# Optimization experiments

Hardware: AMD Instinct MI355X
Metric: run time of the kernel (lower is better)

Reference implementation:

```python
import jax, jax.numpy as jnp
import numpy as np

B, S, D, H = 8, 2048, 1024, 64

def setup_inputs() -> dict:
    key = jax.random.key(0)
    ks = jax.random.split(key, 7)
    scale = 0.02
    return {
        "x": jax.random.normal(ks[0], (B, S, D), dtype=jnp.float32),
        "Wq": jax.random.normal(ks[1], (D, H), dtype=jnp.float32) * scale,
        "bq": jax.random.normal(ks[2], (H,), dtype=jnp.float32) * scale,
        "Wk": jax.random.normal(ks[3], (D, H), dtype=jnp.float32) * scale,
        "bk": jax.random.normal(ks[4], (H,), dtype=jnp.float32) * scale,
        "Wv": jax.random.normal(ks[5], (D, H), dtype=jnp.float32) * scale,
        "bv": jax.random.normal(ks[6], (H,), dtype=jnp.float32) * scale,
    }

def reference(x, Wq, bq, Wk, bk, Wv, bv):
    # Single-head causal self-attention (dropout in eval mode -> identity).
    q = x @ Wq + bq            # [B,S,H]
    k = x @ Wk + bk            # [B,S,H]
    v = x @ Wv + bv            # [B,S,H]
    scores = jnp.einsum("bqh,bkh->bqk", q, k)  # [B,S,S]
    s = q.shape[1]
    causal = jnp.tril(jnp.ones((s, s), dtype=bool))
    # Original masks with -inf BEFORE scaling; -inf/scale == -inf, so equivalent.
    scores = jnp.where(causal, scores, -jnp.inf) / jnp.sqrt(jnp.float32(k.shape[-1]))
    attn = jax.nn.softmax(scores, axis=-1)
    return jnp.einsum("bqk,bkh->bqh", attn, v)
```

## Files before the change

### kernel.cpp

```cpp
#include <hip/hip_runtime.h>
#include <math.h>

#define BATCH 8
#define SEQ   2048
#define DIM   1024
#define HD    64
#define NROWS (BATCH * SEQ)
#define CHUNK 256
#define NCHUNK 8
#define QTILE 64
#define NQT   (SEQ / QTILE)
#define QSCALE 0.1803368801f

typedef __attribute__((ext_vector_type(8))) short bf16x8;
typedef __attribute__((ext_vector_type(4))) float f32x4;

__device__ __forceinline__ unsigned short f2bf(float f) {
    unsigned u = __float_as_uint(f);
    u = (u + 0x7FFFu + ((u >> 16) & 1u)) >> 16;
    return (unsigned short)u;
}
__device__ __forceinline__ unsigned short f2bf_hu(float f) {
    return (unsigned short)((__float_as_uint(f) + 0x8000u) >> 16);
}
__device__ __forceinline__ float fast_exp2(float x) {
#if __has_builtin(__builtin_amdgcn_exp2f)
    return __builtin_amdgcn_exp2f(x);
#else
    return exp2f(x);
#endif
}

__device__ __forceinline__ void gld_lds16(const void* g, void* l) {
    __builtin_amdgcn_global_load_lds(
        (const __attribute__((address_space(1))) void*)g,
        (__attribute__((address_space(3))) void*)l, 16, 0, 0);
}


__global__ __launch_bounds__(256)
void prep_w_kernel(const float* __restrict__ Wq, const float* __restrict__ Wk,
                   const float* __restrict__ Wv, unsigned short* __restrict__ Wt)
{
    const int mat = blockIdx.y;
    const float* __restrict__ W = (mat == 0) ? Wq : (mat == 1) ? Wk : Wv;
    const int k0 = blockIdx.x * 64;
    __shared__ float T[64][65];
    const int t = threadIdx.x;
    #pragma unroll
    for (int i = 0; i < 16; ++i) {
        const int idx = t + i * 256;
        T[idx >> 6][idx & 63] = W[(size_t)(k0 + (idx >> 6)) * HD + (idx & 63)];
    }
    __syncthreads();
    const int n = t >> 2;
    const int c = t & 3;
    union { unsigned short h[16]; uint4 v[2]; } buf;
    #pragma unroll
    for (int j = 0; j < 16; ++j) buf.h[j] = f2bf(T[c * 16 + j][n]);
    unsigned short* dst = Wt + ((size_t)mat * HD + n) * DIM + k0 + c * 16;
    *(uint4*)dst       = buf.v[0];
    *(uint4*)(dst + 8) = buf.v[1];
}

__global__ __launch_bounds__(384)
void qkv_mfma_kernel(const float* __restrict__ x,
                     const unsigned short* __restrict__ Wt,
                     const float* __restrict__ bq, const float* __restrict__ bk,
                     const float* __restrict__ bv,
                     unsigned short* __restrict__ Qg,
                     unsigned short* __restrict__ Kg,
                     unsigned short* __restrict__ Vtg)
{
    __shared__ unsigned short Xs[32][128];
    __shared__ unsigned short Ws[192][128];

    const int t    = threadIdx.x;
    const int lane = t & 63;
    const int w    = t >> 6;
    const int col  = lane & 15;
    const int quad = lane >> 4;
    const int rh   = w & 1;
    const int mat  = w >> 1;
    const int row0 = blockIdx.x * 32;

    const int r4   = lane >> 4;
    const int ch16 = lane & 15;

    f32x4 acc[4];
    #pragma unroll
    for (int i = 0; i < 4; ++i) acc[i] = (f32x4){0.f, 0.f, 0.f, 0.f};

    const int xr  = t >> 3;
    const int xc0 = t & 7;
    const float* __restrict__ xrow = &x[(size_t)(row0 + xr) * DIM];
    float4 xv[4];
    if (t < 256) {
        xv[0] = *(const float4*)(xrow + xc0 * 8);
        xv[1] = *(const float4*)(xrow + xc0 * 8 + 4);
        xv[2] = *(const float4*)(xrow + (xc0 + 8) * 8);
        xv[3] = *(const float4*)(xrow + (xc0 + 8) * 8 + 4);
    }

    for (int it = 0; it < 8; ++it) {
        const int k0 = it * 128;
        __syncthreads();
        if (t < 256) {
            #pragma unroll
            for (int h = 0; h < 2; ++h) {
                const int g = xc0 + h * 8;
                const float4 v0 = xv[h * 2];
                const float4 v1 = xv[h * 2 + 1];
                uint4 o;
                o.x = ((__float_as_uint(v0.x) + 0x8000u) >> 16) | ((__float_as_uint(v0.y) + 0x8000u) & 0xFFFF0000u);
                o.y = ((__float_as_uint(v0.z) + 0x8000u) >> 16) | ((__float_as_uint(v0.w) + 0x8000u) & 0xFFFF0000u);
                o.z = ((__float_as_uint(v1.x) + 0x8000u) >> 16) | ((__float_as_uint(v1.y) + 0x8000u) & 0xFFFF0000u);
                o.w = ((__float_as_uint(v1.z) + 0x8000u) >> 16) | ((__float_as_uint(v1.w) + 0x8000u) & 0xFFFF0000u);
                *(uint4*)&Xs[xr][(g ^ (xr & 15)) * 8] = o;
            }
        }
        #pragma unroll
        for (int ii = 0; ii < 8; ++ii) {
            const int rbase = w * 32 + ii * 4;
            const int r = rbase + r4;
            gld_lds16(&Wt[(size_t)r * DIM + k0 + (ch16 ^ (r & 15)) * 8], &Ws[rbase][0]);
        }
        __syncthreads();
        if (it < 7 && t < 256) {
            const float* xp = xrow + k0 + 128;
            xv[0] = *(const float4*)(xp + xc0 * 8);
            xv[1] = *(const float4*)(xp + xc0 * 8 + 4);
            xv[2] = *(const float4*)(xp + (xc0 + 8) * 8);
            xv[3] = *(const float4*)(xp + (xc0 + 8) * 8 + 4);
        }
        #pragma unroll
        for (int ks = 0; ks < 4; ++ks) {
            const int fswz = ((ks * 4 + quad) ^ col) * 8;
            const bf16x8 a = *(const bf16x8*)&Xs[rh * 16 + col][fswz];
            #pragma unroll
            for (int nt = 0; nt < 4; ++nt) {
                const bf16x8 b = *(const bf16x8*)&Ws[mat * 64 + nt * 16 + col][fswz];
                acc[nt] = __builtin_amdgcn_mfma_f32_16x16x32_bf16(a, b, acc[nt], 0, 0, 0);
            }
        }
    }

    const int b    = row0 / SEQ;
    const int s0   = (row0 % SEQ) + rh * 16 + quad * 4;
    const int grow = row0 + rh * 16 + quad * 4;
    const float* __restrict__ bias = (mat == 0) ? bq : (mat == 1) ? bk : bv;
    const float oscale = (mat == 0) ? QSCALE : 1.0f;
    #pragma unroll
    for (int nt = 0; nt < 4; ++nt) {
        const int nn = nt * 16 + col;
        const float bvv = bias[nn];
        if (mat < 2) {
            unsigned short* __restrict__ o = (mat == 0) ? Qg : Kg;
            #pragma unroll
            for (int r = 0; r < 4; ++r)
                o[(size_t)(grow + r) * HD + nn] = f2bf((acc[nt][r] + bvv) * oscale);
        } else {
            const unsigned lo = (unsigned)f2bf(acc[nt][0] + bvv) | ((unsigned)f2bf(acc[nt][1] + bvv) << 16);
            const unsigned hi = (unsigned)f2bf(acc[nt][2] + bvv) | ((unsigned)f2bf(acc[nt][3] + bvv) << 16);
            *(uint2*)&Vtg[((size_t)b * HD + nn) * SEQ + s0] = make_uint2(lo, hi);
        }
    }
}

__global__ __launch_bounds__(256)
void attn_part_kernel(const unsigned short* __restrict__ Qg,
                      const unsigned short* __restrict__ Kg,
                      const unsigned short* __restrict__ Vtg,
                      unsigned short* __restrict__ Opart,
                      float* __restrict__ Lsum)
{
    const int b = blockIdx.x;
    int y = blockIdx.y, c = 0;
    while (y >= 32 - 4 * c) { y -= 32 - 4 * c; ++c; }
    const int qt = y + 4 * c;

    __shared__ unsigned short Ks[64][64];
    __shared__ unsigned short Vs[64][64];
    __shared__ unsigned short Ps[4][16][76];

    const int t    = threadIdx.x;
    const int w    = t >> 6;
    const int lane = t & 63;
    const int col  = lane & 15;
    const int quad = lane >> 4;
    const int q0w  = qt * QTILE + w * 16;
    const size_t gq = (size_t)b * SEQ + q0w;

    const bf16x8 aq0 = *(const bf16x8*)&Qg[(gq + col) * HD + quad * 8];
    const bf16x8 aq1 = *(const bf16x8*)&Qg[(gq + col) * HD + 32 + quad * 8];

    f32x4 oacc[4];
    #pragma unroll
    for (int n = 0; n < 4; ++n) oacc[n] = (f32x4){0.f, 0.f, 0.f, 0.f};
    float lpart[4] = {0.f, 0.f, 0.f, 0.f};

    const int kbeg   = c * CHUNK;
    const int kend   = min((c + 1) * CHUNK, (qt + 1) * QTILE);
    const int ntiles = (kend - kbeg + 63) >> 6;

    const int r8 = lane >> 3, ch = lane & 7;
    const int swzr = (ch ^ r8) * 8;
    const unsigned short* kgb = Kg  + (size_t)b * SEQ * HD;
    const unsigned short* vgb = Vtg + (size_t)b * HD * SEQ;

    for (int it = 0; it < ntiles; ++it) {
        const int j0 = kbeg + it * 64;
        __syncthreads();
        #pragma unroll
        for (int ii = 0; ii < 2; ++ii) {
            const int rb = w * 16 + ii * 8;
            gld_lds16(&kgb[(size_t)(j0 + rb + r8) * HD + swzr], &Ks[rb][0]);
            gld_lds16(&vgb[(size_t)(rb + r8) * SEQ + j0 + swzr], &Vs[rb][0]);
        }
        __syncthreads();

        if (j0 <= q0w + 15) {
            f32x4 scv[4];
            #pragma unroll
            for (int nt = 0; nt < 4; ++nt) {
                const int sw0 = (quad ^ (col & 7)) * 8;
                const int sw1 = ((4 + quad) ^ (col & 7)) * 8;
                const bf16x8 bk0 = *(const bf16x8*)&Ks[nt * 16 + col][sw0];
                const bf16x8 bk1 = *(const bf16x8*)&Ks[nt * 16 + col][sw1];
                f32x4 s = __builtin_amdgcn_mfma_f32_16x16x32_bf16(aq0, bk0, (f32x4){0.f,0.f,0.f,0.f}, 0, 0, 0);
                s = __builtin_amdgcn_mfma_f32_16x16x32_bf16(aq1, bk1, s, 0, 0, 0);
                scv[nt] = s;
            }
            const bool needmask = (j0 + 63 > q0w);
            #pragma unroll
            for (int r = 0; r < 4; ++r) {
                const int row = q0w + quad * 4 + r;
                #pragma unroll
                for (int nt = 0; nt < 4; ++nt) {
                    float s = scv[nt][r];
                    if (needmask)
                        s = (j0 + nt * 16 + col <= row) ? s : -INFINITY;
                    const float p = fast_exp2(s);
                    lpart[r] += p;
                    Ps[w][quad * 4 + r][nt * 16 + col] = f2bf_hu(p);
                }
            }
            #pragma unroll
            for (int ks = 0; ks < 2; ++ks) {
                const bf16x8 ap = *(const bf16x8*)&Ps[w][col][ks * 32 + quad * 8];
                const int fswz = ((ks * 4 + quad) ^ (col & 7)) * 8;
                #pragma unroll
                for (int n = 0; n < 4; ++n) {
                    const bf16x8 bv2 = *(const bf16x8*)&Vs[n * 16 + col][fswz];
                    oacc[n] = __builtin_amdgcn_mfma_f32_16x16x32_bf16(ap, bv2, oacc[n], 0, 0, 0);
                }
            }
        }
    }

    #pragma unroll
    for (int r = 0; r < 4; ++r) {
        #pragma unroll
        for (int off = 1; off < 16; off <<= 1)
            lpart[r] += __shfl_xor(lpart[r], off, 64);
    }

    const int blk = (b * NQT + qt) * NCHUNK + c;
    unsigned short* Ob = Opart + (size_t)blk * (QTILE * HD);
    #pragma unroll
    for (int n = 0; n < 4; ++n)
        #pragma unroll
        for (int r = 0; r < 4; ++r)
            Ob[(w * 16 + quad * 4 + r) * HD + n * 16 + col] = f2bf(oacc[n][r]);
    if (col == 0) {
        float* lb = Lsum + (size_t)blk * QTILE;
        #pragma unroll
        for (int r = 0; r < 4; ++r)
            lb[w * 16 + quad * 4 + r] = lpart[r];
    }
}

__global__ __launch_bounds__(256)
void combine_kernel(const unsigned short* __restrict__ Opart,
                    const float* __restrict__ Lsum,
                    float* __restrict__ out)
{
    const int gid = blockIdx.x * 256 + threadIdx.x;
    const int i   = gid >> 4;
    const int d4  = (gid & 15) * 4;
    const int b   = i >> 11;
    const int s   = i & 2047;
    const int qt  = s >> 6;
    const int r64 = s & 63;
    const int nc  = (s >> 8) + 1;
    const int blk0 = (b * NQT + qt) * NCHUNK;

    float L = 0.f;
    float a0 = 0.f, a1 = 0.f, a2 = 0.f, a3 = 0.f;
    for (int cc = 0; cc < nc; ++cc) {
        L += Lsum[(size_t)(blk0 + cc) * QTILE + r64];
        const uint2 u = *(const uint2*)(Opart + (size_t)(blk0 + cc) * (QTILE * HD) + r64 * HD + d4);
        a0 += __uint_as_float(u.x << 16);
        a1 += __uint_as_float(u.x & 0xFFFF0000u);
        a2 += __uint_as_float(u.y << 16);
        a3 += __uint_as_float(u.y & 0xFFFF0000u);
    }
    const float rL = 1.0f / L;
    float4 o; o.x = a0 * rL; o.y = a1 * rL; o.z = a2 * rL; o.w = a3 * rL;
    *(float4*)&out[(size_t)i * HD + d4] = o;
}

extern "C" void kernel_launch(void* const* d_in, const int* in_sizes, int n_in,
                              void* d_out, int out_size, void* d_ws, size_t ws_size,
                              hipStream_t stream) {
    const float* x  = (const float*)d_in[0];
    const float* Wq = (const float*)d_in[1];
    const float* bq = (const float*)d_in[2];
    const float* Wk = (const float*)d_in[3];
    const float* bk = (const float*)d_in[4];
    const float* Wv = (const float*)d_in[5];
    const float* bv = (const float*)d_in[6];
    float* out = (float*)d_out;

    unsigned short* Wt    = (unsigned short*)d_ws;
    unsigned short* Qg    = Wt + (size_t)3 * HD * DIM;
    unsigned short* Kg    = Qg + (size_t)NROWS * HD;
    unsigned short* Vtg   = Kg + (size_t)NROWS * HD;
    unsigned short* Opart = Vtg + (size_t)BATCH * HD * SEQ;
    float* Lsum = (float*)(Opart + (size_t)BATCH * NQT * NCHUNK * QTILE * HD);

    prep_w_kernel<<<dim3(16, 3), 256, 0, stream>>>(Wq, Wk, Wv, Wt);
    qkv_mfma_kernel<<<dim3(NROWS / 32), 384, 0, stream>>>(x, Wt, bq, bk, bv, Qg, Kg, Vtg);
    attn_part_kernel<<<dim3(8, 144), 256, 0, stream>>>(Qg, Kg, Vtg, Opart, Lsum);
    combine_kernel<<<dim3(NROWS * 16 / 256), 256, 0, stream>>>(Opart, Lsum, out);
}
```

Before: 145.2 us.

## Fuse split-K combine into attention via float atomics and last-block finalize

Drops the separate combine kernel. Each chunk block now atomically adds its unnormalized output and row sums into a zeroed fp32 accumulator, and a per-query-tile counter picks the last arriving block to normalize and write the output. Zeroing of the accumulator is folded into the QKV projection kernel. This removes a launch and the bf16 partial round-trip, but adds many global float atomics and a threadfence per block, and makes the summation order nondeterministic.

```diff
diff --git a/kernel.cpp b/kernel.cpp
--- a/kernel.cpp
+++ b/kernel.cpp
@@ -70,7 +70,9 @@
                      const float* __restrict__ bv,
                      unsigned short* __restrict__ Qg,
                      unsigned short* __restrict__ Kg,
-                     unsigned short* __restrict__ Vtg)
+                     unsigned short* __restrict__ Vtg,
+                     float* __restrict__ Oacc,
+                     unsigned* __restrict__ Cnt)
 {
     __shared__ unsigned short Xs[32][128];
     __shared__ unsigned short Ws[192][128];
@@ -165,14 +167,23 @@
             *(uint2*)&Vtg[((size_t)b * HD + nn) * SEQ + s0] = make_uint2(lo, hi);
         }
     }
+
+    const float4 z4 = (float4){0.f, 0.f, 0.f, 0.f};
+    const int nz = (NROWS * HD + NROWS) / 4;
+    for (int i = blockIdx.x * 384 + t; i < nz; i += 512 * 384)
+        ((float4*)Oacc)[i] = z4;
+    if (blockIdx.x == 0 && t < BATCH * NQT)
+        Cnt[t] = 0u;
 }
 
 __global__ __launch_bounds__(256)
 void attn_part_kernel(const unsigned short* __restrict__ Qg,
                       const unsigned short* __restrict__ Kg,
                       const unsigned short* __restrict__ Vtg,
-                      unsigned short* __restrict__ Opart,
-                      float* __restrict__ Lsum)
+                      float* __restrict__ Oacc,
+                      float* __restrict__ Lacc,
+                      unsigned* __restrict__ Cnt,
+                      float* __restrict__ out)
 {
     const int b = blockIdx.x;
     int y = blockIdx.y, c = 0;
@@ -182,6 +193,7 @@
     __shared__ unsigned short Ks[64][64];
     __shared__ unsigned short Vs[64][64];
     __shared__ unsigned short Ps[4][16][76];
+    __shared__ int isLast;
 
     const int t    = threadIdx.x;
     const int w    = t >> 6;
@@ -265,49 +277,48 @@
             lpart[r] += __shfl_xor(lpart[r], off, 64);
     }
 
-    const int blk = (b * NQT + qt) * NCHUNK + c;
-    unsigned short* Ob = Opart + (size_t)blk * (QTILE * HD);
+    const int qrow0 = qt * QTILE;
+    float* __restrict__ Ob = Oacc + ((size_t)b * SEQ + qrow0) * HD;
     #pragma unroll
     for (int n = 0; n < 4; ++n)
         #pragma unroll
         for (int r = 0; r < 4; ++r)
-            Ob[(w * 16 + quad * 4 + r) * HD + n * 16 + col] = f2bf(oacc[n][r]);
+            atomicAdd(&Ob[(w * 16 + quad * 4 + r) * HD + n * 16 + col], oacc[n][r]);
     if (col == 0) {
-        float* lb = Lsum + (size_t)blk * QTILE;
+        float* lb = Lacc + (size_t)b * SEQ + qrow0 + w * 16;
         #pragma unroll
         for (int r = 0; r < 4; ++r)
-            lb[w * 16 + quad * 4 + r] = lpart[r];
-    }
-}
-
-__global__ __launch_bounds__(256)
-void combine_kernel(const unsigned short* __restrict__ Opart,
-                    const float* __restrict__ Lsum,
-                    float* __restrict__ out)
-{
-    const int gid = blockIdx.x * 256 + threadIdx.x;
-    const int i   = gid >> 4;
-    const int d4  = (gid & 15) * 4;
-    const int b   = i >> 11;
-    const int s   = i & 2047;
-    const int qt  = s >> 6;
-    const int r64 = s & 63;
-    const int nc  = (s >> 8) + 1;
-    const int blk0 = (b * NQT + qt) * NCHUNK;
-
-    float L = 0.f;
-    float a0 = 0.f, a1 = 0.f, a2 = 0.f, a3 = 0.f;
-    for (int cc = 0; cc < nc; ++cc) {
-        L += Lsum[(size_t)(blk0 + cc) * QTILE + r64];
-        const uint2 u = *(const uint2*)(Opart + (size_t)(blk0 + cc) * (QTILE * HD) + r64 * HD + d4);
-        a0 += __uint_as_float(u.x << 16);
-        a1 += __uint_as_float(u.x & 0xFFFF0000u);
-        a2 += __uint_as_float(u.y << 16);
-        a3 += __uint_as_float(u.y & 0xFFFF0000u);
-    }
+            atomicAdd(&lb[quad * 4 + r], lpart[r]);
+    }
+    __threadfence();
+    __syncthreads();
+    if (t == 0) {
+        const int nchunks = (qt >> 2) + 1;
+        isLast = (atomicAdd(&Cnt[b * NQT + qt], 1u) == (unsigned)(nchunks - 1));
+    }
+    __syncthreads();
+    if (!isLast) return;
+
+    const int r   = t >> 2;
+    const int d0  = (t & 3) * 16;
+    const size_t grow = (size_t)b * SEQ + qrow0 + r;
+    const float L = __hip_atomic_load(&Lacc[grow], __ATOMIC_RELAXED,
+                                      __HIP_MEMORY_SCOPE_AGENT);
     const float rL = 1.0f / L;
-    float4 o; o.x = a0 * rL; o.y = a1 * rL; o.z = a2 * rL; o.w = a3 * rL;
-    *(float4*)&out[(size_t)i * HD + d4] = o;
+    float o[16];
+    #pragma unroll
+    for (int j = 0; j < 8; ++j) {
+        const unsigned long long u = __hip_atomic_load(
+            (const unsigned long long*)&Ob[r * HD + d0 + j * 2],
+            __ATOMIC_RELAXED, __HIP_MEMORY_SCOPE_AGENT);
+        o[j * 2]     = __uint_as_float((unsigned)u) * rL;
+        o[j * 2 + 1] = __uint_as_float((unsigned)(u >> 32)) * rL;
+    }
+    float4* op = (float4*)&out[grow * HD + d0];
+    op[0] = (float4){o[0],  o[1],  o[2],  o[3]};
+    op[1] = (float4){o[4],  o[5],  o[6],  o[7]};
+    op[2] = (float4){o[8],  o[9],  o[10], o[11]};
+    op[3] = (float4){o[12], o[13], o[14], o[15]};
 }
 
 extern "C" void kernel_launch(void* const* d_in, const int* in_sizes, int n_in,
@@ -322,15 +333,17 @@
     const float* bv = (const float*)d_in[6];
     float* out = (float*)d_out;
 
-    unsigned short* Wt    = (unsigned short*)d_ws;
-    unsigned short* Qg    = Wt + (size_t)3 * HD * DIM;
-    unsigned short* Kg    = Qg + (size_t)NROWS * HD;
-    unsigned short* Vtg   = Kg + (size_t)NROWS * HD;
-    unsigned short* Opart = Vtg + (size_t)BATCH * HD * SEQ;
-    float* Lsum = (float*)(Opart + (size_t)BATCH * NQT * NCHUNK * QTILE * HD);
+    unsigned short* Wt  = (unsigned short*)d_ws;
+    unsigned short* Qg  = Wt + (size_t)3 * HD * DIM;
+    unsigned short* Kg  = Qg + (size_t)NROWS * HD;
+    unsigned short* Vtg = Kg + (size_t)NROWS * HD;
+    float* Oacc = (float*)(Vtg + (size_t)BATCH * HD * SEQ);
+    float* Lacc = Oacc + (size_t)NROWS * HD;
+    unsigned* Cnt = (unsigned*)(Lacc + NROWS);
 
     prep_w_kernel<<<dim3(16, 3), 256, 0, stream>>>(Wq, Wk, Wv, Wt);
-    qkv_mfma_kernel<<<dim3(NROWS / 32), 384, 0, stream>>>(x, Wt, bq, bk, bv, Qg, Kg, Vtg);
-    attn_part_kernel<<<dim3(8, 144), 256, 0, stream>>>(Qg, Kg, Vtg, Opart, Lsum);
-    combine_kernel<<<dim3(NROWS * 16 / 256), 256, 0, stream>>>(Opart, Lsum, out);
-}
+    qkv_mfma_kernel<<<dim3(NROWS / 32), 384, 0, stream>>>(x, Wt, bq, bk, bv,
+                                                          Qg, Kg, Vtg, Oacc, Cnt);
+    attn_part_kernel<<<dim3(8, 144), 256, 0, stream>>>(Qg, Kg, Vtg,
+                                                       Oacc, Lacc, Cnt, out);
+}
```

Result: slower. 250.5 us (+72.5%).

## Double-buffer QKV projection LDS tiles with K-step 64

Applied to the files above, without the earlier changes.

The QKV projection kernel now keeps two LDS buffers for the X and W tiles and halves the K step from 128 to 64, so the W global-to-LDS loads and X register loads for the next step are issued before the MFMAs on the current buffer. This overlaps memory latency with compute where the old version serialized load, sync and compute. The trade is twice as many iterations, each with two barriers, and a new swizzle pattern for the narrower rows.

```diff
diff --git a/kernel.cpp b/kernel.cpp
--- a/kernel.cpp
+++ b/kernel.cpp
@@ -37,6 +37,15 @@
         (__attribute__((address_space(3))) void*)l, 16, 0, 0);
 }
 
+__device__ __forceinline__ uint4 pack_bf16x8(float4 a, float4 b) {
+    uint4 o;
+    o.x = ((__float_as_uint(a.x) + 0x8000u) >> 16) | ((__float_as_uint(a.y) + 0x8000u) & 0xFFFF0000u);
+    o.y = ((__float_as_uint(a.z) + 0x8000u) >> 16) | ((__float_as_uint(a.w) + 0x8000u) & 0xFFFF0000u);
+    o.z = ((__float_as_uint(b.x) + 0x8000u) >> 16) | ((__float_as_uint(b.y) + 0x8000u) & 0xFFFF0000u);
+    o.w = ((__float_as_uint(b.z) + 0x8000u) >> 16) | ((__float_as_uint(b.w) + 0x8000u) & 0xFFFF0000u);
+    return o;
+}
+
 
 __global__ __launch_bounds__(256)
 void prep_w_kernel(const float* __restrict__ Wq, const float* __restrict__ Wk,
@@ -72,8 +81,8 @@
                      unsigned short* __restrict__ Kg,
                      unsigned short* __restrict__ Vtg)
 {
-    __shared__ unsigned short Xs[32][128];
-    __shared__ unsigned short Ws[192][128];
+    __shared__ unsigned short Xs[2][32][64];
+    __shared__ unsigned short Ws[2][192][64];
 
     const int t    = threadIdx.x;
     const int lane = t & 63;
@@ -84,8 +93,9 @@
     const int mat  = w >> 1;
     const int row0 = blockIdx.x * 32;
 
-    const int r4   = lane >> 4;
-    const int ch16 = lane & 15;
+    const int r8  = lane >> 3;
+    const int ch8 = lane & 7;
+    const int wswz = (ch8 ^ r8) * 8;
 
     f32x4 acc[4];
     #pragma unroll
@@ -94,55 +104,50 @@
     const int xr  = t >> 3;
     const int xc0 = t & 7;
     const float* __restrict__ xrow = &x[(size_t)(row0 + xr) * DIM];
-    float4 xv[4];
+
+    #pragma unroll
+    for (int ii = 0; ii < 4; ++ii) {
+        const int rbase = w * 32 + ii * 8;
+        gld_lds16(&Wt[(size_t)(rbase + r8) * DIM + wswz], &Ws[0][rbase][0]);
+    }
+    float4 xa, xb;
     if (t < 256) {
-        xv[0] = *(const float4*)(xrow + xc0 * 8);
-        xv[1] = *(const float4*)(xrow + xc0 * 8 + 4);
-        xv[2] = *(const float4*)(xrow + (xc0 + 8) * 8);
-        xv[3] = *(const float4*)(xrow + (xc0 + 8) * 8 + 4);
-    }
-
-    for (int it = 0; it < 8; ++it) {
-        const int k0 = it * 128;
+        xa = *(const float4*)(xrow + xc0 * 8);
+        xb = *(const float4*)(xrow + xc0 * 8 + 4);
+        *(uint4*)&Xs[0][xr][(xc0 ^ (xr & 7)) * 8] = pack_bf16x8(xa, xb);
+    }
+    __syncthreads();
+
+    int buf = 0;
+    for (int it = 0; it < 16; ++it) {
+        if (it < 15) {
+            const int k0n = (it + 1) * 64;
+            #pragma unroll
+            for (int ii = 0; ii < 4; ++ii) {
+                const int rbase = w * 32 + ii * 8;
+                gld_lds16(&Wt[(size_t)(rbase + r8) * DIM + k0n + wswz],
+                          &Ws[buf ^ 1][rbase][0]);
+            }
+            if (t < 256) {
+                xa = *(const float4*)(xrow + k0n + xc0 * 8);
+                xb = *(const float4*)(xrow + k0n + xc0 * 8 + 4);
+            }
+        }
+        #pragma unroll
+        for (int ks = 0; ks < 2; ++ks) {
+            const int fswz = ((ks * 4 + quad) ^ (col & 7)) * 8;
+            const bf16x8 a = *(const bf16x8*)&Xs[buf][rh * 16 + col][fswz];
+            #pragma unroll
+            for (int nt = 0; nt < 4; ++nt) {
+                const bf16x8 b = *(const bf16x8*)&Ws[buf][mat * 64 + nt * 16 + col][fswz];
+                acc[nt] = __builtin_amdgcn_mfma_f32_16x16x32_bf16(a, b, acc[nt], 0, 0, 0);
+            }
+        }
         __syncthreads();
-        if (t < 256) {
-            #pragma unroll
-            for (int h = 0; h < 2; ++h) {
-                const int g = xc0 + h * 8;
-                const float4 v0 = xv[h * 2];
-                const float4 v1 = xv[h * 2 + 1];
-                uint4 o;
-                o.x = ((__float_as_uint(v0.x) + 0x8000u) >> 16) | ((__float_as_uint(v0.y) + 0x8000u) & 0xFFFF0000u);
-                o.y = ((__float_as_uint(v0.z) + 0x8000u) >> 16) | ((__float_as_uint(v0.w) + 0x8000u) & 0xFFFF0000u);
-                o.z = ((__float_as_uint(v1.x) + 0x8000u) >> 16) | ((__float_as_uint(v1.y) + 0x8000u) & 0xFFFF0000u);
-                o.w = ((__float_as_uint(v1.z) + 0x8000u) >> 16) | ((__float_as_uint(v1.w) + 0x8000u) & 0xFFFF0000u);
-                *(uint4*)&Xs[xr][(g ^ (xr & 15)) * 8] = o;
-            }
-        }
-        #pragma unroll
-        for (int ii = 0; ii < 8; ++ii) {
-            const int rbase = w * 32 + ii * 4;
-            const int r = rbase + r4;
-            gld_lds16(&Wt[(size_t)r * DIM + k0 + (ch16 ^ (r & 15)) * 8], &Ws[rbase][0]);
-        }
+        if (it < 15 && t < 256)
+            *(uint4*)&Xs[buf ^ 1][xr][(xc0 ^ (xr & 7)) * 8] = pack_bf16x8(xa, xb);
         __syncthreads();
-        if (it < 7 && t < 256) {
-            const float* xp = xrow + k0 + 128;
-            xv[0] = *(const float4*)(xp + xc0 * 8);
-            xv[1] = *(const float4*)(xp + xc0 * 8 + 4);
-            xv[2] = *(const float4*)(xp + (xc0 + 8) * 8);
-            xv[3] = *(const float4*)(xp + (xc0 + 8) * 8 + 4);
-        }
-        #pragma unroll
-        for (int ks = 0; ks < 4; ++ks) {
-            const int fswz = ((ks * 4 + quad) ^ col) * 8;
-            const bf16x8 a = *(const bf16x8*)&Xs[rh * 16 + col][fswz];
-            #pragma unroll
-            for (int nt = 0; nt < 4; ++nt) {
-                const bf16x8 b = *(const bf16x8*)&Ws[mat * 64 + nt * 16 + col][fswz];
-                acc[nt] = __builtin_amdgcn_mfma_f32_16x16x32_bf16(a, b, acc[nt], 0, 0, 0);
-            }
-        }
+        buf ^= 1;
     }
 
     const int b    = row0 / SEQ;
```

New measurement: 151.4 us. +4.3%, slower.
